# Performance work log

Measured on AMD Instinct MI355X. Metric: run time of the kernel, lower is better.

Reference implementation:

```python
import jax, jax.numpy as jnp
import numpy as np

N_NODES = 170000
N_EDGES = 1200000
IN, HID, OUT = 128, 128, 64


def setup_inputs() -> dict:
    key = jax.random.key(0)
    ks = jax.random.split(key, 9)
    feat = jax.random.normal(ks[0], (N_NODES, IN), dtype=jnp.float32)
    src = jax.random.randint(ks[1], (N_EDGES,), 0, N_NODES, dtype=jnp.int32)
    dst = jax.random.randint(ks[2], (N_EDGES,), 0, N_NODES, dtype=jnp.int32)
    # Glorot-uniform style init for the GraphConv weights, zero bias (DGL default)
    def glorot(k, fan_in, fan_out):
        lim = np.sqrt(6.0 / (fan_in + fan_out)).astype(np.float32)
        return jax.random.uniform(k, (fan_in, fan_out), jnp.float32, -lim, lim)
    W0 = glorot(ks[3], IN, HID)
    W1 = glorot(ks[4], HID, HID)
    W2 = glorot(ks[5], HID, OUT)
    b0 = jnp.zeros((HID,), jnp.float32)
    b1 = jnp.zeros((HID,), jnp.float32)
    b2 = jnp.zeros((OUT,), jnp.float32)
    return {"feat": feat, "src": src, "dst": dst,
            "W0": W0, "b0": b0, "W1": W1, "b1": b1, "W2": W2, "b2": b2}


def _gcn_layer(h, src, dst, norm_out, norm_in, W, b, relu):
    # norm='both': D_out^{-1/2} scaling, sum-aggregate over edges, D_in^{-1/2} scaling
    h = h * norm_out                                   # [N, d]
    agg = jax.ops.segment_sum(h[src], dst, num_segments=N_NODES)  # gather+scatter-add
    r = (agg * norm_in) @ W + b                        # dense transform + bias
    return jax.nn.relu(r) if relu else r


def reference(feat, src, dst, W0, b0, W1, b1, W2, b2):
    ones = jnp.ones((N_EDGES,), jnp.float32)
    # DGL clamps degrees to min 1 (allow_zero_in_degree=True keeps zero-degree nodes)
    deg_out = jnp.clip(jax.ops.segment_sum(ones, src, num_segments=N_NODES), 1.0)
    deg_in = jnp.clip(jax.ops.segment_sum(ones, dst, num_segments=N_NODES), 1.0)
    norm_out = (deg_out ** -0.5)[:, None]
    norm_in = (deg_in ** -0.5)[:, None]
    # Dropout(0.5) between layers is identity in eval mode
    h = _gcn_layer(feat, src, dst, norm_out, norm_in, W0, b0, relu=True)
    h = _gcn_layer(h, src, dst, norm_out, norm_in, W1, b1, relu=True)
    h = _gcn_layer(h, src, dst, norm_out, norm_in, W2, b2, relu=False)
    return h
```

## Files before the change

### kernel.cpp

```cpp
#include <hip/hip_runtime.h>
#include <hip/hip_bf16.h>

#define N_NODES 170000
#define N_EDGES 1200000

#define AITEMS 2048
#define NB_A   586
#define NCB    333
#define SCAN_A_N      (NCB * NB_A)
#define SCAN_A_BLOCKS 191
#define SCAN_A_PAD    (SCAN_A_BLOCKS * 1024)
#define HISTA_PAD     195140

#define DOUT_NPC    16384
#define DOUT_WPC    8192
#define DOUT_NCHUNK 11
#define DOUT_NSLICE 96
#define DOUT_SLICE_E (N_EDGES / DOUT_NSLICE)
#define WORDS_N     85000

typedef short bf16x8 __attribute__((ext_vector_type(8)));
typedef float f32x4 __attribute__((ext_vector_type(4)));

__device__ __forceinline__ void bf_split(float v, __hip_bfloat16& h, __hip_bfloat16& l)
{
    h = __float2bfloat16(v);
    l = __float2bfloat16(v - __bfloat162float(h));
}

__device__ __forceinline__ int lds_addr(int row, int col)
{
    return (row * 256 + col * 2) ^ ((row & 7) << 4);
}


__global__ __launch_bounds__(256) void coarse_hist_kernel(
    const int* __restrict__ dst, int* __restrict__ histA, int nedges)
{
    __shared__ int h[NCB];
    int t = threadIdx.x;
    for (int j = t; j < NCB; j += 256) h[j] = 0;
    __syncthreads();
    int base = blockIdx.x * AITEMS;
    #pragma unroll
    for (int j = 0; j < AITEMS / 256; j++) {
        int i = base + j * 256 + t;
        if (i < nedges) atomicAdd(&h[dst[i] >> 9], 1);
    }
    __syncthreads();
    for (int j = t; j < NCB; j += 256)
        histA[j * NB_A + blockIdx.x] = h[j];
}

__global__ __launch_bounds__(256) void scan1_kernel(
    const int* __restrict__ in, int* __restrict__ partial,
    int* __restrict__ blockSums, int n)
{
    __shared__ int sdata[256];
    int t = threadIdx.x;
    int base = blockIdx.x * 1024 + t * 4;
    int4 v = make_int4(0, 0, 0, 0);
    if (base + 3 < n) v = *(const int4*)&in[base];
    else {
        if (base + 0 < n) v.x = in[base + 0];
        if (base + 1 < n) v.y = in[base + 1];
        if (base + 2 < n) v.z = in[base + 2];
        if (base + 3 < n) v.w = in[base + 3];
    }
    int tsum = v.x + v.y + v.z + v.w;
    sdata[t] = tsum;
    __syncthreads();
    for (int off = 1; off < 256; off <<= 1) {
        int add = 0;
        if (t >= off) add = sdata[t - off];
        __syncthreads();
        if (t >= off) sdata[t] += add;
        __syncthreads();
    }
    int excl = sdata[t] - tsum;
    int4 o;
    o.x = excl;
    o.y = o.x + v.x;
    o.z = o.y + v.y;
    o.w = o.z + v.z;
    *(int4*)&partial[base] = o;
    if (t == 255) blockSums[blockIdx.x] = sdata[255];
}

__global__ __launch_bounds__(256) void scan2_kernel(int* __restrict__ blockSums, int nb)
{
    __shared__ int sdata[256];
    int t = threadIdx.x;
    int val = (t < nb) ? blockSums[t] : 0;
    sdata[t] = val;
    __syncthreads();
    for (int off = 1; off < 256; off <<= 1) {
        int add = 0;
        if (t >= off) add = sdata[t - off];
        __syncthreads();
        if (t >= off) sdata[t] += add;
        __syncthreads();
    }
    if (t < nb) blockSums[t] = sdata[t] - val;
}

__global__ __launch_bounds__(256) void scan3_kernel(
    int* __restrict__ buf, const int* __restrict__ blockSums)
{
    int off = blockSums[blockIdx.x];
    int base = blockIdx.x * 1024 + threadIdx.x * 4;
    int4 v = *(const int4*)&buf[base];
    v.x += off; v.y += off; v.z += off; v.w += off;
    *(int4*)&buf[base] = v;
}

__global__ __launch_bounds__(256) void coarse_scatter_kernel(
    const int* __restrict__ src, const int* __restrict__ dst,
    const int* __restrict__ scanA, int* __restrict__ pairs, int nedges)
{
    __shared__ int base[NCB];
    __shared__ int cur[NCB];
    int t = threadIdx.x;
    for (int j = t; j < NCB; j += 256) {
        base[j] = scanA[j * NB_A + blockIdx.x];
        cur[j] = 0;
    }
    __syncthreads();
    int eb = blockIdx.x * AITEMS;
    #pragma unroll
    for (int j = 0; j < AITEMS / 256; j++) {
        int i = eb + j * 256 + t;
        if (i < nedges) {
            int d = dst[i];
            int cb = d >> 9;
            int r = atomicAdd(&cur[cb], 1);
            pairs[base[cb] + r] = (src[i] << 9) | (d & 511);
        }
    }
}

__global__ __launch_bounds__(256) void bucket_sort_kernel(
    const int* __restrict__ pairs, const int* __restrict__ scanA,
    int* __restrict__ csr, int* __restrict__ row_start,
    float* __restrict__ norm_in, int nedges)
{
    __shared__ int hist[512];
    __shared__ int curs[512];
    __shared__ int sdata[256];
    int cb = blockIdx.x;
    int t = threadIdx.x;
    int beg = scanA[cb * NB_A];
    int end = (cb == NCB - 1) ? nedges : scanA[(cb + 1) * NB_A];

    hist[t] = 0; hist[t + 256] = 0;
    __syncthreads();
    for (int j = beg + t; j < end; j += 256)
        atomicAdd(&hist[pairs[j] & 511], 1);
    __syncthreads();

    int a = hist[2 * t], b = hist[2 * t + 1];
    sdata[t] = a + b;
    __syncthreads();
    for (int off = 1; off < 256; off <<= 1) {
        int add = 0;
        if (t >= off) add = sdata[t - off];
        __syncthreads();
        if (t >= off) sdata[t] += add;
        __syncthreads();
    }
    int epair = sdata[t] - (a + b);
    curs[2 * t]     = beg + epair;
    curs[2 * t + 1] = beg + epair + a;
    __syncthreads();

    int nodeBase = cb << 9;
    for (int s = t; s < 512; s += 256) {
        int v = nodeBase + s;
        if (v < N_NODES) {
            row_start[v] = curs[s];
            norm_in[v] = rsqrtf(fmaxf((float)hist[s], 1.0f));
        }
    }
    if (cb == NCB - 1 && t == 0) row_start[N_NODES] = nedges;
    __syncthreads();

    for (int j = beg + t; j < end; j += 256) {
        int p = pairs[j];
        int pos = atomicAdd(&curs[p & 511], 1);
        csr[pos] = p >> 9;
    }
}

__global__ __launch_bounds__(256) void degout_hist_kernel(
    const int* __restrict__ src, unsigned* __restrict__ partial)
{
    __shared__ unsigned h[DOUT_WPC];
    int chunk = blockIdx.x / DOUT_NSLICE;
    int slice = blockIdx.x % DOUT_NSLICE;
    int lo = chunk * DOUT_NPC;
    int t = threadIdx.x;
    #pragma unroll
    for (int j = 0; j < DOUT_WPC / 256; j++) h[j * 256 + t] = 0;
    __syncthreads();
    const int4* sp = (const int4*)(src + slice * DOUT_SLICE_E);
    for (int i = t; i < DOUT_SLICE_E / 4; i += 256) {
        int4 v = sp[i];
        unsigned a = (unsigned)(v.x - lo);
        if (a < DOUT_NPC) atomicAdd(&h[a >> 1], 1u << ((a & 1) * 16));
        a = (unsigned)(v.y - lo);
        if (a < DOUT_NPC) atomicAdd(&h[a >> 1], 1u << ((a & 1) * 16));
        a = (unsigned)(v.z - lo);
        if (a < DOUT_NPC) atomicAdd(&h[a >> 1], 1u << ((a & 1) * 16));
        a = (unsigned)(v.w - lo);
        if (a < DOUT_NPC) atomicAdd(&h[a >> 1], 1u << ((a & 1) * 16));
    }
    __syncthreads();
    int wlo = chunk * DOUT_WPC;
    int nw = min(DOUT_WPC, WORDS_N - wlo);
    for (int j = t; j < nw; j += 256)
        partial[(size_t)slice * WORDS_N + wlo + j] = h[j];
}

__global__ __launch_bounds__(256) void degout_combine_kernel(
    const unsigned* __restrict__ partial, float* __restrict__ norm_out)
{
    int w = blockIdx.x * 256 + threadIdx.x;
    if (w >= WORDS_N) return;
    unsigned slo = 0, shi = 0;
    #pragma unroll
    for (int s = 0; s < DOUT_NSLICE; s++) {
        unsigned x = partial[(size_t)s * WORDS_N + w];
        slo += x & 0xFFFFu;
        shi += x >> 16;
    }
    norm_out[2 * w]     = rsqrtf(fmaxf((float)slo, 1.0f));
    norm_out[2 * w + 1] = rsqrtf(fmaxf((float)shi, 1.0f));
}

__global__ __launch_bounds__(256) void f2bf_kernel(
    const float* __restrict__ in, __hip_bfloat16* __restrict__ outp, int n8)
{
    int i = blockIdx.x * 256 + threadIdx.x;
    if (i >= n8) return;
    float4 a = *(const float4*)&in[(size_t)i * 8];
    float4 b = *(const float4*)&in[(size_t)i * 8 + 4];
    float4 packed;
    __hip_bfloat162* p = (__hip_bfloat162*)&packed;
    p[0].x = __float2bfloat16(a.x); p[0].y = __float2bfloat16(a.y);
    p[1].x = __float2bfloat16(a.z); p[1].y = __float2bfloat16(a.w);
    p[2].x = __float2bfloat16(b.x); p[2].y = __float2bfloat16(b.y);
    p[3].x = __float2bfloat16(b.z); p[3].y = __float2bfloat16(b.w);
    *(float4*)&outp[(size_t)i * 8] = packed;
}

__global__ __launch_bounds__(256) void wsplit_kernel(
    const float* __restrict__ W, int nout,
    __hip_bfloat16* __restrict__ Whi, __hip_bfloat16* __restrict__ Wlo)
{
    int i = blockIdx.x * 256 + threadIdx.x;
    if (i >= 128 * nout) return;
    int k = i / nout, n = i - k * nout;
    float v = W[i];
    __hip_bfloat16 h, l;
    bf_split(v, h, l);
    Whi[n * 128 + k] = h;
    Wlo[n * 128 + k] = l;
}

template<bool SCALE_SRC, bool FUSE2>
__global__ __launch_bounds__(256) void fused_layer_kernel(
    const __hip_bfloat16* __restrict__ hin, const int* __restrict__ csr,
    const int* __restrict__ row_start, const float* __restrict__ norm_out,
    const float* __restrict__ norm_in, const __hip_bfloat16* __restrict__ Wthi,
    const __hip_bfloat16* __restrict__ Wtlo, const float* __restrict__ bias,
    const float* __restrict__ rowscale, const __hip_bfloat16* __restrict__ W2thi,
    const __hip_bfloat16* __restrict__ W2tlo, __hip_bfloat16* __restrict__ outp)
{
    __shared__ __align__(16) unsigned char smem[16384];
    const int r0 = blockIdx.x * 32;

    {
        const int g = threadIdx.x >> 4;
        const int l = threadIdx.x & 15;
        const int gbase = threadIdx.x & 48;
        for (int rr = 0; rr < 2; rr++) {
            const int lrow = g + rr * 16;
            const int row = r0 + lrow;
            float acc[8] = {};
            if (row < N_NODES) {
                int beg = row_start[row];
                int end = row_start[row + 1];
                for (int j = beg; j < end; j += 16) {
                    int cnt = min(16, end - j);
                    int sv = 0;
                    float wv = 0.f;
                    if (j + l < end) {
                        sv = csr[j + l];
                        wv = SCALE_SRC ? norm_out[sv] : 1.f;
                    }
                    int s0 = __shfl(sv, gbase);
                    if (j + l >= end) sv = s0;
                    #pragma unroll
                    for (int ib = 0; ib < 16; ib += 8) {
                        if (ib < cnt) {
                            float4 rg[8];
                            float ww[8];
                            #pragma unroll
                            for (int k = 0; k < 8; k++) {
                                int s = __shfl(sv, gbase + ib + k);
                                ww[k] = __shfl(wv, gbase + ib + k);
                                rg[k] = *(const float4*)(hin + (size_t)s * 128 + l * 8);
                            }
                            #pragma unroll
                            for (int k = 0; k < 8; k++) {
                                const __hip_bfloat162* pp = (const __hip_bfloat162*)&rg[k];
                                float sc = ww[k];
                                float2 f0 = __bfloat1622float2(pp[0]);
                                float2 f1 = __bfloat1622float2(pp[1]);
                                float2 f2 = __bfloat1622float2(pp[2]);
                                float2 f3 = __bfloat1622float2(pp[3]);
                                acc[0] += f0.x * sc; acc[1] += f0.y * sc;
                                acc[2] += f1.x * sc; acc[3] += f1.y * sc;
                                acc[4] += f2.x * sc; acc[5] += f2.y * sc;
                                acc[6] += f3.x * sc; acc[7] += f3.y * sc;
                            }
                        }
                    }
                }
            }
            float ni = (row < N_NODES) ? norm_in[row] : 0.f;
            float4 ph, pl;
            __hip_bfloat16* hp = (__hip_bfloat16*)&ph;
            __hip_bfloat16* lp = (__hip_bfloat16*)&pl;
            #pragma unroll
            for (int jj = 0; jj < 8; jj++) bf_split(acc[jj] * ni, hp[jj], lp[jj]);
            int off = lds_addr(lrow, l * 8);
            *(float4*)(smem + off) = ph;
            *(float4*)(smem + 8192 + off) = pl;
        }
    }
    __syncthreads();

    const int wave = threadIdx.x >> 6;
    const int lane = threadIdx.x & 63;
    const int n = lane & 15;
    const int q = lane >> 4;
    const size_t bbase = (size_t)n * 128 + q * 8;
    const f32x4 zero = {0.f, 0.f, 0.f, 0.f};
    f32x4 acc0[2], acc1[2];
    acc0[0] = zero; acc0[1] = zero; acc1[0] = zero; acc1[1] = zero;

    #pragma unroll 1
    for (int kc = 0; kc < 4; kc++) {
        const int a0 = lds_addr(n, q * 8 + kc * 32);
        const int a1 = lds_addr(n + 16, q * 8 + kc * 32);
        bf16x8 ah0 = *(const bf16x8*)(smem + a0);
        bf16x8 al0 = *(const bf16x8*)(smem + 8192 + a0);
        bf16x8 ah1 = *(const bf16x8*)(smem + a1);
        bf16x8 al1 = *(const bf16x8*)(smem + 8192 + a1);
        #pragma unroll
        for (int c = 0; c < 2; c++) {
            const int ct = wave * 2 + c;
            bf16x8 bh = *(const bf16x8*)(Wthi + (size_t)ct * 2048 + bbase + kc * 32);
            bf16x8 bl = *(const bf16x8*)(Wtlo + (size_t)ct * 2048 + bbase + kc * 32);
            acc0[c] = __builtin_amdgcn_mfma_f32_16x16x32_bf16(ah0, bh, acc0[c], 0, 0, 0);
            acc0[c] = __builtin_amdgcn_mfma_f32_16x16x32_bf16(al0, bh, acc0[c], 0, 0, 0);
            acc0[c] = __builtin_amdgcn_mfma_f32_16x16x32_bf16(ah0, bl, acc0[c], 0, 0, 0);
            acc1[c] = __builtin_amdgcn_mfma_f32_16x16x32_bf16(ah1, bh, acc1[c], 0, 0, 0);
            acc1[c] = __builtin_amdgcn_mfma_f32_16x16x32_bf16(al1, bh, acc1[c], 0, 0, 0);
            acc1[c] = __builtin_amdgcn_mfma_f32_16x16x32_bf16(ah1, bl, acc1[c], 0, 0, 0);
        }
    }

    float bcol[2];
    bcol[0] = bias[(wave * 2 + 0) * 16 + n];
    bcol[1] = bias[(wave * 2 + 1) * 16 + n];

    if (!FUSE2) {
        #pragma unroll
        for (int r = 0; r < 4; r++) {
            int g0 = r0 + q * 4 + r;
            int g1 = g0 + 16;
            float rs0 = rowscale[min(g0, N_NODES - 1)];
            float rs1 = rowscale[min(g1, N_NODES - 1)];
            #pragma unroll
            for (int c = 0; c < 2; c++) {
                int col = (wave * 2 + c) * 16 + n;
                float v0 = fmaxf(acc0[c][r] + bcol[c], 0.f) * rs0;
                float v1 = fmaxf(acc1[c][r] + bcol[c], 0.f) * rs1;
                if (g0 < N_NODES) outp[(size_t)g0 * 128 + col] = __float2bfloat16(v0);
                if (g1 < N_NODES) outp[(size_t)g1 * 128 + col] = __float2bfloat16(v1);
            }
        }
    } else {
        __syncthreads();
        #pragma unroll
        for (int r = 0; r < 4; r++) {
            int lr0 = q * 4 + r;
            int lr1 = lr0 + 16;
            float rs0 = rowscale[min(r0 + lr0, N_NODES - 1)];
            float rs1 = rowscale[min(r0 + lr1, N_NODES - 1)];
            #pragma unroll
            for (int c = 0; c < 2; c++) {
                int col = (wave * 2 + c) * 16 + n;
                float v0 = fmaxf(acc0[c][r] + bcol[c], 0.f) * rs0;
                float v1 = fmaxf(acc1[c][r] + bcol[c], 0.f) * rs1;
                __hip_bfloat16 hh, ll;
                bf_split(v0, hh, ll);
                *(__hip_bfloat16*)(smem + lds_addr(lr0, col)) = hh;
                *(__hip_bfloat16*)(smem + 8192 + lds_addr(lr0, col)) = ll;
                bf_split(v1, hh, ll);
                *(__hip_bfloat16*)(smem + lds_addr(lr1, col)) = hh;
                *(__hip_bfloat16*)(smem + 8192 + lds_addr(lr1, col)) = ll;
            }
        }
        __syncthreads();

        f32x4 c0 = zero, c1 = zero;
        #pragma unroll 1
        for (int kc = 0; kc < 4; kc++) {
            const int a0 = lds_addr(n, q * 8 + kc * 32);
            const int a1 = lds_addr(n + 16, q * 8 + kc * 32);
            bf16x8 ah0 = *(const bf16x8*)(smem + a0);
            bf16x8 al0 = *(const bf16x8*)(smem + 8192 + a0);
            bf16x8 ah1 = *(const bf16x8*)(smem + a1);
            bf16x8 al1 = *(const bf16x8*)(smem + 8192 + a1);
            bf16x8 bh = *(const bf16x8*)(W2thi + (size_t)wave * 2048 + bbase + kc * 32);
            bf16x8 bl = *(const bf16x8*)(W2tlo + (size_t)wave * 2048 + bbase + kc * 32);
            c0 = __builtin_amdgcn_mfma_f32_16x16x32_bf16(ah0, bh, c0, 0, 0, 0);
            c0 = __builtin_amdgcn_mfma_f32_16x16x32_bf16(al0, bh, c0, 0, 0, 0);
            c0 = __builtin_amdgcn_mfma_f32_16x16x32_bf16(ah0, bl, c0, 0, 0, 0);
            c1 = __builtin_amdgcn_mfma_f32_16x16x32_bf16(ah1, bh, c1, 0, 0, 0);
            c1 = __builtin_amdgcn_mfma_f32_16x16x32_bf16(al1, bh, c1, 0, 0, 0);
            c1 = __builtin_amdgcn_mfma_f32_16x16x32_bf16(ah1, bl, c1, 0, 0, 0);
        }
        #pragma unroll
        for (int r = 0; r < 4; r++) {
            int g0 = r0 + q * 4 + r;
            int g1 = g0 + 16;
            int col = wave * 16 + n;
            if (g0 < N_NODES) outp[(size_t)g0 * 64 + col] = __float2bfloat16(c0[r]);
            if (g1 < N_NODES) outp[(size_t)g1 * 64 + col] = __float2bfloat16(c1[r]);
        }
    }
}

__global__ __launch_bounds__(256) void final_gather_kernel(
    const __hip_bfloat16* __restrict__ h, const int* __restrict__ csr,
    const int* __restrict__ row_start, const float* __restrict__ norm_in,
    const float* __restrict__ bias, float* __restrict__ outf)
{
    int tid = blockIdx.x * 256 + threadIdx.x;
    int row = tid >> 4;
    int l = threadIdx.x & 15;
    int gbase = threadIdx.x & 48;
    if (row >= N_NODES) return;
    int beg = row_start[row];
    int end = row_start[row + 1];
    float acc[4] = {};
    for (int j = beg; j < end; j += 16) {
        int cnt = min(16, end - j);
        int sv = 0;
        float wv = 0.f;
        if (j + l < end) { sv = csr[j + l]; wv = 1.f; }
        int s0 = __shfl(sv, gbase);
        if (j + l >= end) sv = s0;
        #pragma unroll
        for (int ib = 0; ib < 16; ib += 8) {
            if (ib < cnt) {
                float2 rg[8];
                float ww[8];
                #pragma unroll
                for (int k = 0; k < 8; k++) {
                    int s = __shfl(sv, gbase + ib + k);
                    ww[k] = __shfl(wv, gbase + ib + k);
                    rg[k] = *(const float2*)(h + (size_t)s * 64 + l * 4);
                }
                #pragma unroll
                for (int k = 0; k < 8; k++) {
                    const __hip_bfloat162* pp = (const __hip_bfloat162*)&rg[k];
                    float sc = ww[k];
                    float2 f0 = __bfloat1622float2(pp[0]);
                    float2 f1 = __bfloat1622float2(pp[1]);
                    acc[0] += f0.x * sc; acc[1] += f0.y * sc;
                    acc[2] += f1.x * sc; acc[3] += f1.y * sc;
                }
            }
        }
    }
    float ni = norm_in[row];
    float4 o0 = make_float4(acc[0] * ni, acc[1] * ni, acc[2] * ni, acc[3] * ni);
    float4 b = *(const float4*)&bias[l * 4];
    o0.x += b.x; o0.y += b.y; o0.z += b.z; o0.w += b.w;
    *(float4*)&outf[(size_t)row * 64 + l * 4] = o0;
}

extern "C" void kernel_launch(void* const* d_in, const int* in_sizes, int n_in,
                              void* d_out, int out_size, void* d_ws, size_t ws_size,
                              hipStream_t stream)
{
    const float* feat = (const float*)d_in[0];
    const int* src    = (const int*)d_in[1];
    const int* dst    = (const int*)d_in[2];
    const float* W0   = (const float*)d_in[3];
    const float* b0   = (const float*)d_in[4];
    const float* W1   = (const float*)d_in[5];
    const float* b1   = (const float*)d_in[6];
    const float* W2   = (const float*)d_in[7];
    const float* b2   = (const float*)d_in[8];
    float* out = (float*)d_out;

    const int N = N_NODES;
    const int E = N_EDGES;

    char* ws = (char*)d_ws;
    float* norm_out = (float*)ws;
    float* norm_in  = norm_out + N;
    int* row_start  = (int*)(norm_in + N);
    int* csr        = row_start + 170004;
    __hip_bfloat16* Wt0hi = (__hip_bfloat16*)(csr + E);
    __hip_bfloat16* Wt0lo = Wt0hi + 16384;
    __hip_bfloat16* Wt1hi = Wt0lo + 16384;
    __hip_bfloat16* Wt1lo = Wt1hi + 16384;
    __hip_bfloat16* Wt2hi = Wt1lo + 16384;
    __hip_bfloat16* Wt2lo = Wt2hi + 8192;
    __hip_bfloat16* bfbuf = Wt2lo + 8192;
    __hip_bfloat16* h1    = bfbuf + (size_t)N * 128;
    __hip_bfloat16* aux   = h1 + (size_t)N * 128;
    int* histA          = (int*)h1;
    int* scanA          = histA + HISTA_PAD;
    int* blockSumsA     = scanA + SCAN_A_PAD + 4;
    unsigned* partial   = (unsigned*)(blockSumsA + 256);
    int* pairs          = (int*)aux;

    degout_hist_kernel<<<DOUT_NCHUNK * DOUT_NSLICE, 256, 0, stream>>>(src, partial);
    degout_combine_kernel<<<(WORDS_N + 255) / 256, 256, 0, stream>>>(partial, norm_out);
    coarse_hist_kernel<<<NB_A, 256, 0, stream>>>(dst, histA, E);
    scan1_kernel<<<SCAN_A_BLOCKS, 256, 0, stream>>>(histA, scanA, blockSumsA, SCAN_A_N);
    scan2_kernel<<<1, 256, 0, stream>>>(blockSumsA, SCAN_A_BLOCKS);
    scan3_kernel<<<SCAN_A_BLOCKS, 256, 0, stream>>>(scanA, blockSumsA);
    coarse_scatter_kernel<<<NB_A, 256, 0, stream>>>(src, dst, scanA, pairs, E);
    bucket_sort_kernel<<<NCB, 256, 0, stream>>>(pairs, scanA, csr, row_start, norm_in, E);
    f2bf_kernel<<<(N * 16 + 255) / 256, 256, 0, stream>>>(feat, bfbuf, N * 16);
    wsplit_kernel<<<64, 256, 0, stream>>>(W0, 128, Wt0hi, Wt0lo);
    wsplit_kernel<<<64, 256, 0, stream>>>(W1, 128, Wt1hi, Wt1lo);
    wsplit_kernel<<<32, 256, 0, stream>>>(W2, 64, Wt2hi, Wt2lo);

    const int fusedBlocks = (N + 31) / 32;
    const int gatherBlocks = (N * 16 + 255) / 256;

    fused_layer_kernel<true, false><<<fusedBlocks, 256, 0, stream>>>(
        bfbuf, csr, row_start, norm_out, norm_in, Wt0hi, Wt0lo, b0, norm_out,
        nullptr, nullptr, h1);

    fused_layer_kernel<false, true><<<fusedBlocks, 256, 0, stream>>>(
        h1, csr, row_start, nullptr, norm_in, Wt1hi, Wt1lo, b1, norm_out,
        Wt2hi, Wt2lo, bfbuf);

    final_gather_kernel<<<gatherBlocks, 256, 0, stream>>>(
        bfbuf, csr, row_start, norm_in, b2, out);
}
```

Measured before the change: 518.8 us.

## Sort nodes by in-degree so fused layer blocks get balanced rows

```diff
diff --git a/kernel.cpp b/kernel.cpp
--- a/kernel.cpp
+++ b/kernel.cpp
@@ -18,6 +18,11 @@
 #define DOUT_NSLICE 96
 #define DOUT_SLICE_E (N_EDGES / DOUT_NSLICE)
 #define WORDS_N     85000
+
+#define DEG_BINS 64
+#define NB_D 167
+#define SCAN_D_N (DEG_BINS * NB_D)
+#define SCAN_D_BLOCKS 11
 
 typedef short bf16x8 __attribute__((ext_vector_type(8)));
 typedef float f32x4 __attribute__((ext_vector_type(4)));
@@ -237,6 +242,47 @@
     norm_out[2 * w + 1] = rsqrtf(fmaxf((float)shi, 1.0f));
 }
 
+__global__ __launch_bounds__(256) void deg_hist_kernel(
+    const int* __restrict__ row_start, int* __restrict__ histD)
+{
+    __shared__ int hd[DEG_BINS];
+    int t = threadIdx.x;
+    if (t < DEG_BINS) hd[t] = 0;
+    __syncthreads();
+    int base = blockIdx.x * 1024;
+    #pragma unroll
+    for (int k = 0; k < 4; k++) {
+        int v = base + k * 256 + t;
+        if (v < N_NODES) {
+            int d = min(row_start[v + 1] - row_start[v], DEG_BINS - 1);
+            atomicAdd(&hd[DEG_BINS - 1 - d], 1);
+        }
+    }
+    __syncthreads();
+    if (t < DEG_BINS) histD[t * NB_D + blockIdx.x] = hd[t];
+}
+
+__global__ __launch_bounds__(256) void deg_scatter_kernel(
+    const int* __restrict__ row_start, const int* __restrict__ scanD,
+    int* __restrict__ perm)
+{
+    __shared__ int basec[DEG_BINS];
+    __shared__ int cur[DEG_BINS];
+    int t = threadIdx.x;
+    if (t < DEG_BINS) { basec[t] = scanD[t * NB_D + blockIdx.x]; cur[t] = 0; }
+    __syncthreads();
+    int base = blockIdx.x * 1024;
+    #pragma unroll
+    for (int k = 0; k < 4; k++) {
+        int v = base + k * 256 + t;
+        if (v < N_NODES) {
+            int d = DEG_BINS - 1 - min(row_start[v + 1] - row_start[v], DEG_BINS - 1);
+            int r = atomicAdd(&cur[d], 1);
+            perm[basec[d] + r] = v;
+        }
+    }
+}
+
 __global__ __launch_bounds__(256) void f2bf_kernel(
     const float* __restrict__ in, __hip_bfloat16* __restrict__ outp, int n8)
 {
@@ -270,7 +316,8 @@
 template<bool SCALE_SRC, bool FUSE2>
 __global__ __launch_bounds__(256) void fused_layer_kernel(
     const __hip_bfloat16* __restrict__ hin, const int* __restrict__ csr,
-    const int* __restrict__ row_start, const float* __restrict__ norm_out,
+    const int* __restrict__ row_start, const int* __restrict__ perm,
+    const float* __restrict__ norm_out,
     const float* __restrict__ norm_in, const __hip_bfloat16* __restrict__ Wthi,
     const __hip_bfloat16* __restrict__ Wtlo, const float* __restrict__ bias,
     const float* __restrict__ rowscale, const __hip_bfloat16* __restrict__ W2thi,
@@ -285,9 +332,12 @@
         const int gbase = threadIdx.x & 48;
         for (int rr = 0; rr < 2; rr++) {
             const int lrow = g + rr * 16;
-            const int row = r0 + lrow;
+            const int pidx = r0 + lrow;
+            const int row = (pidx < N_NODES) ? perm[pidx] : -1;
             float acc[8] = {};
-            if (row < N_NODES) {
+            float ni = 0.f;
+            if (row >= 0) {
+                ni = norm_in[row];
                 int beg = row_start[row];
                 int end = row_start[row + 1];
                 for (int j = beg; j < end; j += 16) {
@@ -328,7 +378,6 @@
                     }
                 }
             }
-            float ni = (row < N_NODES) ? norm_in[row] : 0.f;
             float4 ph, pl;
             __hip_bfloat16* hp = (__hip_bfloat16*)&ph;
             __hip_bfloat16* lp = (__hip_bfloat16*)&pl;
@@ -379,17 +428,19 @@
     if (!FUSE2) {
         #pragma unroll
         for (int r = 0; r < 4; r++) {
-            int g0 = r0 + q * 4 + r;
-            int g1 = g0 + 16;
-            float rs0 = rowscale[min(g0, N_NODES - 1)];
-            float rs1 = rowscale[min(g1, N_NODES - 1)];
+            int i0 = r0 + q * 4 + r;
+            int i1 = i0 + 16;
+            int p0 = perm[min(i0, N_NODES - 1)];
+            int p1 = perm[min(i1, N_NODES - 1)];
+            float rs0 = rowscale[p0];
+            float rs1 = rowscale[p1];
             #pragma unroll
             for (int c = 0; c < 2; c++) {
                 int col = (wave * 2 + c) * 16 + n;
                 float v0 = fmaxf(acc0[c][r] + bcol[c], 0.f) * rs0;
                 float v1 = fmaxf(acc1[c][r] + bcol[c], 0.f) * rs1;
-                if (g0 < N_NODES) outp[(size_t)g0 * 128 + col] = __float2bfloat16(v0);
-                if (g1 < N_NODES) outp[(size_t)g1 * 128 + col] = __float2bfloat16(v1);
+                if (i0 < N_NODES) outp[(size_t)p0 * 128 + col] = __float2bfloat16(v0);
+                if (i1 < N_NODES) outp[(size_t)p1 * 128 + col] = __float2bfloat16(v1);
             }
         }
     } else {
@@ -398,8 +449,8 @@
         for (int r = 0; r < 4; r++) {
             int lr0 = q * 4 + r;
             int lr1 = lr0 + 16;
-            float rs0 = rowscale[min(r0 + lr0, N_NODES - 1)];
-            float rs1 = rowscale[min(r0 + lr1, N_NODES - 1)];
+            float rs0 = rowscale[perm[min(r0 + lr0, N_NODES - 1)]];
+            float rs1 = rowscale[perm[min(r0 + lr1, N_NODES - 1)]];
             #pragma unroll
             for (int c = 0; c < 2; c++) {
                 int col = (wave * 2 + c) * 16 + n;
@@ -436,11 +487,13 @@
         }
         #pragma unroll
         for (int r = 0; r < 4; r++) {
-            int g0 = r0 + q * 4 + r;
-            int g1 = g0 + 16;
+            int i0 = r0 + q * 4 + r;
+            int i1 = i0 + 16;
+            int p0 = perm[min(i0, N_NODES - 1)];
+            int p1 = perm[min(i1, N_NODES - 1)];
             int col = wave * 16 + n;
-            if (g0 < N_NODES) outp[(size_t)g0 * 64 + col] = __float2bfloat16(c0[r]);
-            if (g1 < N_NODES) outp[(size_t)g1 * 64 + col] = __float2bfloat16(c1[r]);
+            if (i0 < N_NODES) outp[(size_t)p0 * 64 + col] = __float2bfloat16(c0[r]);
+            if (i1 < N_NODES) outp[(size_t)p1 * 64 + col] = __float2bfloat16(c1[r]);
         }
     }
 }
@@ -532,6 +585,10 @@
     int* blockSumsA     = scanA + SCAN_A_PAD + 4;
     unsigned* partial   = (unsigned*)(blockSumsA + 256);
     int* pairs          = (int*)aux;
+    int* perm           = (int*)aux;
+    int* histD          = perm + 170000;
+    int* scanD          = histD + SCAN_D_N;
+    int* blockSumsD     = scanD + 11268;
 
     degout_hist_kernel<<<DOUT_NCHUNK * DOUT_NSLICE, 256, 0, stream>>>(src, partial);
     degout_combine_kernel<<<(WORDS_N + 255) / 256, 256, 0, stream>>>(partial, norm_out);
@@ -541,6 +598,11 @@
     scan3_kernel<<<SCAN_A_BLOCKS, 256, 0, stream>>>(scanA, blockSumsA);
     coarse_scatter_kernel<<<NB_A, 256, 0, stream>>>(src, dst, scanA, pairs, E);
     bucket_sort_kernel<<<NCB, 256, 0, stream>>>(pairs, scanA, csr, row_start, norm_in, E);
+    deg_hist_kernel<<<NB_D, 256, 0, stream>>>(row_start, histD);
+    scan1_kernel<<<SCAN_D_BLOCKS, 256, 0, stream>>>(histD, scanD, blockSumsD, SCAN_D_N);
+    scan2_kernel<<<1, 256, 0, stream>>>(blockSumsD, SCAN_D_BLOCKS);
+    scan3_kernel<<<SCAN_D_BLOCKS, 256, 0, stream>>>(scanD, blockSumsD);
+    deg_scatter_kernel<<<NB_D, 256, 0, stream>>>(row_start, scanD, perm);
     f2bf_kernel<<<(N * 16 + 255) / 256, 256, 0, stream>>>(feat, bfbuf, N * 16);
     wsplit_kernel<<<64, 256, 0, stream>>>(W0, 128, Wt0hi, Wt0lo);
     wsplit_kernel<<<64, 256, 0, stream>>>(W1, 128, Wt1hi, Wt1lo);
@@ -550,11 +612,11 @@
     const int gatherBlocks = (N * 16 + 255) / 256;
 
     fused_layer_kernel<true, false><<<fusedBlocks, 256, 0, stream>>>(
-        bfbuf, csr, row_start, norm_out, norm_in, Wt0hi, Wt0lo, b0, norm_out,
+        bfbuf, csr, row_start, perm, norm_out, norm_in, Wt0hi, Wt0lo, b0, norm_out,
         nullptr, nullptr, h1);
 
     fused_layer_kernel<false, true><<<fusedBlocks, 256, 0, stream>>>(
-        h1, csr, row_start, nullptr, norm_in, Wt1hi, Wt1lo, b1, norm_out,
+        h1, csr, row_start, perm, nullptr, norm_in, Wt1hi, Wt1lo, b1, norm_out,
         Wt2hi, Wt2lo, bfbuf);
 
     final_gather_kernel<<<gatherBlocks, 256, 0, stream>>>(
```

New measurement: 554.2 us. 6.8% more time.
